# Kernel optimization log

Measured on AMD Instinct MI355X. Metric: run time of the kernel, lower is better.

Reference implementation:

```python
import jax, jax.numpy as jnp
import numpy as np

N_DB = 200000
D_EMB = 512
N_CLASSES = 10
TOP_K = 32


def setup_inputs() -> dict:
    key = jax.random.key(0)
    k1, k2, k3 = jax.random.split(key, 3)
    x = jax.random.normal(k1, (1, D_EMB), dtype=jnp.float32)
    X_emb = jax.random.normal(k2, (N_DB, D_EMB), dtype=jnp.float32)
    X_cls = jax.random.randint(k3, (N_DB,), 0, N_CLASSES, dtype=jnp.int64)
    return {"x": x, "X_emb": X_emb, "X_cls": X_cls, "k": TOP_K}


def reference(x, X_emb, X_cls, k):
    # Original: for each database row, dist = ||emb - x||_2, keep k smallest
    # (sorted ascending by distance). Fused as cdist (single query) + top_k.
    diff = X_emb - x                      # [N, d] (x broadcasts from [1, d])
    dists = jnp.sqrt(jnp.sum(diff * diff, axis=1))  # [N]
    neg_top, idx = jax.lax.top_k(-dists, k)         # smallest k distances
    nbr_emb = X_emb[idx]                  # [k, d]
    nbr_cls = X_cls[idx]                  # [k]
    nbr_dist = -neg_top                   # [k], ascending
    return nbr_emb, nbr_cls, nbr_dist
```

## Files before the change

kernel.cpp:

```cpp
#include <hip/hip_runtime.h>
#include <float.h>
#include <math.h>

#define N_DB   200000
#define D_EMB  512
#define K      32

#define NBLK   256
#define TPB    512
#define WAVES  (TPB / 64)
#define RPB    ((N_DB + NBLK - 1) / NBLK)
#define NCAND  (NBLK * K)

__global__ __launch_bounds__(TPB) void knn_dist_topk(
    const float* __restrict__ x,
    const float* __restrict__ X_emb,
    float* __restrict__ cand_d,
    int*   __restrict__ cand_i)
{
    __shared__ float xs[D_EMB];
    __shared__ float dists[RPB];
    __shared__ float redv[WAVES];
    __shared__ int   redi[WAVES];

    const int tid  = threadIdx.x;
    const int wid  = tid >> 6;
    const int lane = tid & 63;
    const int base = blockIdx.x * RPB;
    const int rows = min(RPB, N_DB - base);

    for (int i = tid; i < D_EMB; i += TPB) xs[i] = x[i];
    __syncthreads();

    const float4* xq = (const float4*)xs;
    const float4 q0 = xq[lane];
    const float4 q1 = xq[lane + 64];

    for (int r = wid; r < rows; r += WAVES) {
        const float4* p = (const float4*)(X_emb + (size_t)(base + r) * D_EMB);
        float4 a = p[lane];
        float4 b = p[lane + 64];
        float s = 0.f, d;
        d = a.x - q0.x; s = fmaf(d, d, s);
        d = a.y - q0.y; s = fmaf(d, d, s);
        d = a.z - q0.z; s = fmaf(d, d, s);
        d = a.w - q0.w; s = fmaf(d, d, s);
        d = b.x - q1.x; s = fmaf(d, d, s);
        d = b.y - q1.y; s = fmaf(d, d, s);
        d = b.z - q1.z; s = fmaf(d, d, s);
        d = b.w - q1.w; s = fmaf(d, d, s);
        #pragma unroll
        for (int off = 32; off > 0; off >>= 1) s += __shfl_xor(s, off);
        if (lane == 0) dists[r] = sqrtf(s);
    }
    __syncthreads();

    for (int it = 0; it < K; ++it) {
        float bv = FLT_MAX;
        int   bi = 0x7FFFFFFF;
        for (int i = tid; i < rows; i += TPB) {
            float v = dists[i];
            if (v < bv) { bv = v; bi = i; }
        }
        #pragma unroll
        for (int off = 32; off > 0; off >>= 1) {
            float ov = __shfl_xor(bv, off);
            int   oi = __shfl_xor(bi, off);
            if (ov < bv || (ov == bv && oi < bi)) { bv = ov; bi = oi; }
        }
        if (lane == 0) { redv[wid] = bv; redi[wid] = bi; }
        __syncthreads();
        if (tid == 0) {
            float v = redv[0]; int b = redi[0];
            #pragma unroll
            for (int w = 1; w < WAVES; ++w) {
                if (redv[w] < v || (redv[w] == v && redi[w] < b)) {
                    v = redv[w]; b = redi[w];
                }
            }
            cand_d[blockIdx.x * K + it] = v;
            cand_i[blockIdx.x * K + it] = base + b;
            if (b >= 0 && b < rows) dists[b] = FLT_MAX;
        }
        __syncthreads();
    }
}

__global__ __launch_bounds__(256) void knn_final(
    const float* __restrict__ X_emb,
    const int*   __restrict__ X_cls,
    const float* __restrict__ cand_d,
    const int*   __restrict__ cand_i,
    float* __restrict__ out)
{
    __shared__ float cd[NCAND];
    __shared__ float redv[4];
    __shared__ int   redi[4];
    __shared__ int   sel_i[K];
    __shared__ float sel_d[K];

    const int tid  = threadIdx.x;
    const int wid  = tid >> 6;
    const int lane = tid & 63;

    for (int i = tid; i < NCAND; i += 256) cd[i] = cand_d[i];
    __syncthreads();

    for (int it = 0; it < K; ++it) {
        float bv = FLT_MAX;
        int   bi = 0x7FFFFFFF;
        for (int i = tid; i < NCAND; i += 256) {
            float v = cd[i];
            if (v < bv) { bv = v; bi = i; }
        }
        #pragma unroll
        for (int off = 32; off > 0; off >>= 1) {
            float ov = __shfl_xor(bv, off);
            int   oi = __shfl_xor(bi, off);
            if (ov < bv || (ov == bv && oi < bi)) { bv = ov; bi = oi; }
        }
        if (lane == 0) { redv[wid] = bv; redi[wid] = bi; }
        __syncthreads();
        if (tid == 0) {
            float v = redv[0]; int b = redi[0];
            #pragma unroll
            for (int w = 1; w < 4; ++w) {
                if (redv[w] < v || (redv[w] == v && redi[w] < b)) {
                    v = redv[w]; b = redi[w];
                }
            }
            sel_d[it] = v;
            sel_i[it] = cand_i[b];
            cd[b] = FLT_MAX;
        }
        __syncthreads();
    }

    float4* out_emb = (float4*)out;
    for (int r = wid; r < K; r += 4) {
        const float4* p = (const float4*)(X_emb + (size_t)sel_i[r] * D_EMB);
        out_emb[r * 128 + lane]      = p[lane];
        out_emb[r * 128 + lane + 64] = p[lane + 64];
    }
    if (tid < K) {
        out[K * D_EMB + tid]     = (float)X_cls[sel_i[tid]];
        out[K * D_EMB + K + tid] = sel_d[tid];
    }
}

extern "C" void kernel_launch(void* const* d_in, const int* in_sizes, int n_in,
                              void* d_out, int out_size, void* d_ws, size_t ws_size,
                              hipStream_t stream) {
    const float* x     = (const float*)d_in[0];
    const float* X_emb = (const float*)d_in[1];
    const int*   X_cls = (const int*)d_in[2];

    float* cand_d = (float*)d_ws;
    int*   cand_i = (int*)((char*)d_ws + NCAND * sizeof(float));

    knn_dist_topk<<<NBLK, TPB, 0, stream>>>(x, X_emb, cand_d, cand_i);
    knn_final<<<1, 256, 0, stream>>>(X_emb, X_cls, cand_d, cand_i, (float*)d_out);
}
```

Measured before the change: 664.0 us.

## Unroll distance loop over four rows per wave and double block count

Each wave now processes a contiguous row range and loads four rows at once with interleaved reductions, raising memory-level parallelism in the bandwidth-bound distance pass. The grid doubles to 512 blocks for better CU occupancy, and the final merge kernel uses 512 threads. In exchange the candidate pool doubles, so the single-block final selection scans twice as many entries per iteration and uses more shared memory.

Measured after the change: 671.9 us. About the same (+1.2%).

```diff
diff --git a/kernel.cpp b/kernel.cpp
--- a/kernel.cpp
+++ b/kernel.cpp
@@ -6,11 +6,14 @@
 #define D_EMB  512
 #define K      32
 
-#define NBLK   256
+#define NBLK   512
 #define TPB    512
 #define WAVES  (TPB / 64)
 #define RPB    ((N_DB + NBLK - 1) / NBLK)
 #define NCAND  (NBLK * K)
+
+#define TPB2   512
+#define WAVES2 (TPB2 / 64)
 
 __global__ __launch_bounds__(TPB) void knn_dist_topk(
     const float* __restrict__ x,
@@ -36,7 +39,69 @@
     const float4 q0 = xq[lane];
     const float4 q1 = xq[lane + 64];
 
-    for (int r = wid; r < rows; r += WAVES) {
+    const int per_wave = (rows + WAVES - 1) / WAVES;
+    const int w0 = min(wid * per_wave, rows);
+    const int w1 = min(w0 + per_wave, rows);
+
+    int r = w0;
+    for (; r + 4 <= w1; r += 4) {
+        const float* rp = X_emb + (size_t)(base + r) * D_EMB;
+        const float4* p0 = (const float4*)(rp);
+        const float4* p1 = (const float4*)(rp + D_EMB);
+        const float4* p2 = (const float4*)(rp + 2 * D_EMB);
+        const float4* p3 = (const float4*)(rp + 3 * D_EMB);
+        float4 a0 = p0[lane], b0 = p0[lane + 64];
+        float4 a1 = p1[lane], b1 = p1[lane + 64];
+        float4 a2 = p2[lane], b2 = p2[lane + 64];
+        float4 a3 = p3[lane], b3 = p3[lane + 64];
+        float s0 = 0.f, s1 = 0.f, s2 = 0.f, s3 = 0.f, d;
+        d = a0.x - q0.x; s0 = fmaf(d, d, s0);
+        d = a0.y - q0.y; s0 = fmaf(d, d, s0);
+        d = a0.z - q0.z; s0 = fmaf(d, d, s0);
+        d = a0.w - q0.w; s0 = fmaf(d, d, s0);
+        d = b0.x - q1.x; s0 = fmaf(d, d, s0);
+        d = b0.y - q1.y; s0 = fmaf(d, d, s0);
+        d = b0.z - q1.z; s0 = fmaf(d, d, s0);
+        d = b0.w - q1.w; s0 = fmaf(d, d, s0);
+        d = a1.x - q0.x; s1 = fmaf(d, d, s1);
+        d = a1.y - q0.y; s1 = fmaf(d, d, s1);
+        d = a1.z - q0.z; s1 = fmaf(d, d, s1);
+        d = a1.w - q0.w; s1 = fmaf(d, d, s1);
+        d = b1.x - q1.x; s1 = fmaf(d, d, s1);
+        d = b1.y - q1.y; s1 = fmaf(d, d, s1);
+        d = b1.z - q1.z; s1 = fmaf(d, d, s1);
+        d = b1.w - q1.w; s1 = fmaf(d, d, s1);
+        d = a2.x - q0.x; s2 = fmaf(d, d, s2);
+        d = a2.y - q0.y; s2 = fmaf(d, d, s2);
+        d = a2.z - q0.z; s2 = fmaf(d, d, s2);
+        d = a2.w - q0.w; s2 = fmaf(d, d, s2);
+        d = b2.x - q1.x; s2 = fmaf(d, d, s2);
+        d = b2.y - q1.y; s2 = fmaf(d, d, s2);
+        d = b2.z - q1.z; s2 = fmaf(d, d, s2);
+        d = b2.w - q1.w; s2 = fmaf(d, d, s2);
+        d = a3.x - q0.x; s3 = fmaf(d, d, s3);
+        d = a3.y - q0.y; s3 = fmaf(d, d, s3);
+        d = a3.z - q0.z; s3 = fmaf(d, d, s3);
+        d = a3.w - q0.w; s3 = fmaf(d, d, s3);
+        d = b3.x - q1.x; s3 = fmaf(d, d, s3);
+        d = b3.y - q1.y; s3 = fmaf(d, d, s3);
+        d = b3.z - q1.z; s3 = fmaf(d, d, s3);
+        d = b3.w - q1.w; s3 = fmaf(d, d, s3);
+        #pragma unroll
+        for (int off = 32; off > 0; off >>= 1) {
+            s0 += __shfl_xor(s0, off);
+            s1 += __shfl_xor(s1, off);
+            s2 += __shfl_xor(s2, off);
+            s3 += __shfl_xor(s3, off);
+        }
+        if (lane == 0) {
+            dists[r]     = sqrtf(s0);
+            dists[r + 1] = sqrtf(s1);
+            dists[r + 2] = sqrtf(s2);
+            dists[r + 3] = sqrtf(s3);
+        }
+    }
+    for (; r < w1; ++r) {
         const float4* p = (const float4*)(X_emb + (size_t)(base + r) * D_EMB);
         float4 a = p[lane];
         float4 b = p[lane + 64];
@@ -86,7 +151,7 @@
     }
 }
 
-__global__ __launch_bounds__(256) void knn_final(
+__global__ __launch_bounds__(TPB2) void knn_final(
     const float* __restrict__ X_emb,
     const int*   __restrict__ X_cls,
     const float* __restrict__ cand_d,
@@ -94,8 +159,8 @@
     float* __restrict__ out)
 {
     __shared__ float cd[NCAND];
-    __shared__ float redv[4];
-    __shared__ int   redi[4];
+    __shared__ float redv[WAVES2];
+    __shared__ int   redi[WAVES2];
     __shared__ int   sel_i[K];
     __shared__ float sel_d[K];
 
@@ -103,13 +168,13 @@
     const int wid  = tid >> 6;
     const int lane = tid & 63;
 
-    for (int i = tid; i < NCAND; i += 256) cd[i] = cand_d[i];
+    for (int i = tid; i < NCAND; i += TPB2) cd[i] = cand_d[i];
     __syncthreads();
 
     for (int it = 0; it < K; ++it) {
         float bv = FLT_MAX;
         int   bi = 0x7FFFFFFF;
-        for (int i = tid; i < NCAND; i += 256) {
+        for (int i = tid; i < NCAND; i += TPB2) {
             float v = cd[i];
             if (v < bv) { bv = v; bi = i; }
         }
@@ -124,7 +189,7 @@
         if (tid == 0) {
             float v = redv[0]; int b = redi[0];
             #pragma unroll
-            for (int w = 1; w < 4; ++w) {
+            for (int w = 1; w < WAVES2; ++w) {
                 if (redv[w] < v || (redv[w] == v && redi[w] < b)) {
                     v = redv[w]; b = redi[w];
                 }
@@ -137,10 +202,10 @@
     }
 
     float4* out_emb = (float4*)out;
-    for (int r = wid; r < K; r += 4) {
-        const float4* p = (const float4*)(X_emb + (size_t)sel_i[r] * D_EMB);
-        out_emb[r * 128 + lane]      = p[lane];
-        out_emb[r * 128 + lane + 64] = p[lane + 64];
+    for (int rr = wid; rr < K; rr += WAVES2) {
+        const float4* p = (const float4*)(X_emb + (size_t)sel_i[rr] * D_EMB);
+        out_emb[rr * 128 + lane]      = p[lane];
+        out_emb[rr * 128 + lane + 64] = p[lane + 64];
     }
     if (tid < K) {
         out[K * D_EMB + tid]     = (float)X_cls[sel_i[tid]];
@@ -159,5 +224,5 @@
     int*   cand_i = (int*)((char*)d_ws + NCAND * sizeof(float));
 
     knn_dist_topk<<<NBLK, TPB, 0, stream>>>(x, X_emb, cand_d, cand_i);
-    knn_final<<<1, 256, 0, stream>>>(X_emb, X_cls, cand_d, cand_i, (float*)d_out);
+    knn_final<<<1, TPB2, 0, stream>>>(X_emb, X_cls, cand_d, cand_i, (float*)d_out);
 }
```
